# Kernel optimization log

Measured on AMD Instinct MI355X. Metric: run time of the kernel, lower is better.

## Reference

```python
import jax, jax.numpy as jnp
import numpy as np

D_MODEL = 1024
NUM_HEADS = 16
D_HEAD = D_MODEL // NUM_HEADS
BATCH = 4
SEQ = 2048
NEG_INF = -1e30


def setup_inputs() -> dict:
    key = jax.random.key(0)
    k_x, k_q, k_k, k_v, k_o = jax.random.split(key, 5)
    scale = 1.0 / np.sqrt(D_MODEL)
    x = jax.random.normal(k_x, (BATCH, SEQ, D_MODEL), dtype=jnp.float32)
    Qw = jax.random.normal(k_q, (D_MODEL, D_MODEL), dtype=jnp.float32) * scale
    Kw = jax.random.normal(k_k, (D_MODEL, D_MODEL), dtype=jnp.float32) * scale
    Vw = jax.random.normal(k_v, (D_MODEL, D_MODEL), dtype=jnp.float32) * scale
    Ow = jax.random.normal(k_o, (D_MODEL, D_MODEL), dtype=jnp.float32) * scale
    padding_mask = jnp.zeros((BATCH, SEQ), dtype=bool)  # True = masked position
    return {"x": x, "Qw": Qw, "Kw": Kw, "Vw": Vw, "Ow": Ow, "padding_mask": padding_mask}


def reference(x, Qw, Kw, Vw, Ow, padding_mask):
    B, S, D = x.shape
    H, dh = NUM_HEADS, D_HEAD
    # torch Linear (no bias): y = x @ W.T
    q = jnp.einsum("bsd,ed->bse", x, Qw).reshape(B, S, H, dh)
    k = jnp.einsum("bsd,ed->bse", x, Kw).reshape(B, S, H, dh)
    v = jnp.einsum("bsd,ed->bse", x, Vw).reshape(B, S, H, dh)
    # scores: [B, H, Sq, Sk]
    score = jnp.einsum("bqhd,bkhd->bhqk", q, k) / jnp.sqrt(jnp.float32(dh))
    # causal mask (masked=True)
    causal = jnp.tril(jnp.ones((S, S), dtype=bool))  # True = keep
    score = jnp.where(causal[None, None, :, :], score, NEG_INF)
    # padding mask: True = masked key position
    score = jnp.where(padding_mask[:, None, None, :], NEG_INF, score)
    attn = jax.nn.softmax(score, axis=-1)  # dropout=0.0 (eval mode)
    ctx = jnp.einsum("bhqk,bkhd->bqhd", attn, v).reshape(B, S, D)
    out = jnp.einsum("bsd,ed->bse", ctx, Ow)
    return out
```

## Files before the change

kernel.cpp:

```cpp
#include <hip/hip_runtime.h>
#include <hip/hip_bf16.h>

typedef __attribute__((ext_vector_type(8))) short short8;
typedef __attribute__((ext_vector_type(4))) float f32x4;

#define MFMA_BF16_16x16x32(a,b,c) __builtin_amdgcn_mfma_f32_16x16x32_bf16((a),(b),(c),0,0,0)

constexpr int B_  = 4;
constexpr int S_  = 2048;
constexpr int H_  = 16;
constexpr int DH_ = 64;
constexpr int D_  = 1024;
constexpr int M_  = B_ * S_;

__device__ __forceinline__ unsigned short f2bf(float f) {
  union { float f; unsigned u; } v; v.f = f;
  unsigned u = v.u;
  u += 0x7fffu + ((u >> 16) & 1u);
  return (unsigned short)(u >> 16);
}

__device__ __forceinline__ short8 cvt8(f32x4 a, f32x4 b) {
  union { __hip_bfloat162 h[4]; short8 s; } u;
  u.h[0] = __float22bfloat162_rn(make_float2(a[0], a[1]));
  u.h[1] = __float22bfloat162_rn(make_float2(a[2], a[3]));
  u.h[2] = __float22bfloat162_rn(make_float2(b[0], b[1]));
  u.h[3] = __float22bfloat162_rn(make_float2(b[2], b[3]));
  return u.s;
}

__global__ __launch_bounds__(256)
void gemm_qkv(const float* __restrict__ x,
              const float* __restrict__ Qw, const float* __restrict__ Kw,
              const float* __restrict__ Vw,
              unsigned short* __restrict__ Qo, unsigned short* __restrict__ Ko,
              unsigned short* __restrict__ VTo) {
  constexpr int BM = 128, BK = 32, LDK = 40;
  __shared__ __align__(16) short As[BM * LDK];
  __shared__ __align__(16) short Bs[BM * LDK];

  const int nb = blockIdx.x;
  const float* W;
  unsigned short* out;
  float scale = 1.0f;
  int epi;
  if (nb < 8)       { W = Qw; out = Qo;  scale = 0.125f; epi = 1; }
  else if (nb < 16) { W = Kw; out = Ko;  epi = 1; }
  else              { W = Vw; out = VTo; epi = 2; }

  const int tid  = threadIdx.x;
  const int lane = tid & 63;
  const int w    = tid >> 6;
  const int quad = lane >> 4;
  const int l16  = lane & 15;
  const int wm   = (w >> 1) * 64;
  const int wn   = (w & 1) * 64;

  const int m0 = blockIdx.y * BM;
  const int n0 = (nb & 7) * 128;

  f32x4 acc[4][4];
  #pragma unroll
  for (int i = 0; i < 4; ++i)
    #pragma unroll
    for (int j = 0; j < 4; ++j)
      acc[i][j] = (f32x4){0.f, 0.f, 0.f, 0.f};

  for (int k0 = 0; k0 < D_; k0 += BK) {
    __syncthreads();
    #pragma unroll
    for (int i = 0; i < 2; ++i) {
      int flat = i * 256 + tid;
      int row  = flat >> 2;
      int col  = (flat & 3) * 8;
      const float* Ap = x + (size_t)(m0 + row) * D_ + k0 + col;
      *(short8*)(&As[row * LDK + col]) = cvt8(*(const f32x4*)Ap, *(const f32x4*)(Ap + 4));
      const float* Wp = W + (size_t)(n0 + row) * D_ + k0 + col;
      *(short8*)(&Bs[row * LDK + col]) = cvt8(*(const f32x4*)Wp, *(const f32x4*)(Wp + 4));
    }
    __syncthreads();

    short8 af[4], bf[4];
    #pragma unroll
    for (int i = 0; i < 4; ++i)
      af[i] = *(const short8*)(&As[(wm + i * 16 + l16) * LDK + quad * 8]);
    #pragma unroll
    for (int j = 0; j < 4; ++j)
      bf[j] = *(const short8*)(&Bs[(wn + j * 16 + l16) * LDK + quad * 8]);
    #pragma unroll
    for (int i = 0; i < 4; ++i)
      #pragma unroll
      for (int j = 0; j < 4; ++j)
        acc[i][j] = MFMA_BF16_16x16x32(af[i], bf[j], acc[i][j]);
  }

  #pragma unroll
  for (int i = 0; i < 4; ++i)
    #pragma unroll
    for (int j = 0; j < 4; ++j)
      #pragma unroll
      for (int r = 0; r < 4; ++r) {
        int m = m0 + wm + i * 16 + quad * 4 + r;
        int n = n0 + wn + j * 16 + l16;
        unsigned short bv = f2bf(acc[i][j][r] * scale);
        int b = m >> 11, s = m & (S_ - 1);
        int h = n >> 6,  d = n & (DH_ - 1);
        if (epi == 1)
          out[((size_t)(b * H_ + h) * S_ + s) * DH_ + d] = bv;
        else
          out[((size_t)(b * H_ + h) * DH_ + d) * S_ + s] = bv;
      }
}

__global__ __launch_bounds__(256)
void gemm_out(const unsigned short* __restrict__ A,
              const float* __restrict__ W,
              float* __restrict__ out) {
  constexpr int BM = 128, BK = 32, LDK = 40;
  __shared__ __align__(16) short As[BM * LDK];
  __shared__ __align__(16) short Bs[BM * LDK];

  const int tid  = threadIdx.x;
  const int lane = tid & 63;
  const int w    = tid >> 6;
  const int quad = lane >> 4;
  const int l16  = lane & 15;
  const int wm   = (w >> 1) * 64;
  const int wn   = (w & 1) * 64;

  const int m0 = blockIdx.y * BM;
  const int n0 = blockIdx.x * 128;

  f32x4 acc[4][4];
  #pragma unroll
  for (int i = 0; i < 4; ++i)
    #pragma unroll
    for (int j = 0; j < 4; ++j)
      acc[i][j] = (f32x4){0.f, 0.f, 0.f, 0.f};

  for (int k0 = 0; k0 < D_; k0 += BK) {
    __syncthreads();
    #pragma unroll
    for (int i = 0; i < 2; ++i) {
      int flat = i * 256 + tid;
      int row  = flat >> 2;
      int col  = (flat & 3) * 8;
      *(short8*)(&As[row * LDK + col]) =
          *(const short8*)(A + (size_t)(m0 + row) * D_ + k0 + col);
      const float* Wp = W + (size_t)(n0 + row) * D_ + k0 + col;
      *(short8*)(&Bs[row * LDK + col]) = cvt8(*(const f32x4*)Wp, *(const f32x4*)(Wp + 4));
    }
    __syncthreads();

    short8 af[4], bf[4];
    #pragma unroll
    for (int i = 0; i < 4; ++i)
      af[i] = *(const short8*)(&As[(wm + i * 16 + l16) * LDK + quad * 8]);
    #pragma unroll
    for (int j = 0; j < 4; ++j)
      bf[j] = *(const short8*)(&Bs[(wn + j * 16 + l16) * LDK + quad * 8]);
    #pragma unroll
    for (int i = 0; i < 4; ++i)
      #pragma unroll
      for (int j = 0; j < 4; ++j)
        acc[i][j] = MFMA_BF16_16x16x32(af[i], bf[j], acc[i][j]);
  }

  #pragma unroll
  for (int i = 0; i < 4; ++i)
    #pragma unroll
    for (int j = 0; j < 4; ++j)
      #pragma unroll
      for (int r = 0; r < 4; ++r) {
        int m = m0 + wm + i * 16 + quad * 4 + r;
        int n = n0 + wn + j * 16 + l16;
        out[(size_t)m * D_ + n] = acc[i][j][r];
      }
}

__global__ __launch_bounds__(256)
void attn(const unsigned short* __restrict__ Q,
          const unsigned short* __restrict__ K,
          const unsigned short* __restrict__ VT,
          const unsigned char* __restrict__ pmask,
          unsigned short* __restrict__ CTX) {
  constexpr int LDP = 72;
  __shared__ __align__(16) short Ps[4 * 32 * LDP];

  const int tid  = threadIdx.x;
  const int lane = tid & 63;
  const int w    = tid >> 6;
  const int quad = lane >> 4;
  const int l16  = lane & 15;

  const int b    = blockIdx.z;
  const int h    = blockIdx.y;
  const int pair = blockIdx.x * 4 + w;

  const unsigned short* Qh = Q  + ((size_t)b * H_ + h) * S_ * DH_;
  const unsigned short* Kh = K  + ((size_t)b * H_ + h) * S_ * DH_;
  const unsigned short* Vh = VT + ((size_t)b * H_ + h) * DH_ * S_;
  const unsigned char* pmb = pmask + (size_t)b * S_;
  unsigned short* CTXb = CTX + (size_t)b * S_ * D_;
  short* Pw = &Ps[w * 32 * LDP];

  for (int half = 0; half < 2; ++half) {
    const int qt = half ? (63 - pair) : pair;
    const int qw = qt * 32;

    short8 qf[2][2];
    #pragma unroll
    for (int i = 0; i < 2; ++i)
      #pragma unroll
      for (int c = 0; c < 2; ++c)
        qf[i][c] = *(const short8*)(Qh + (size_t)(qw + i * 16 + l16) * DH_ + c * 32 + quad * 8);

    f32x4 acc[2][4];
    float mrow[2][4], lrow[2][4];
    #pragma unroll
    for (int i = 0; i < 2; ++i)
      #pragma unroll
      for (int t = 0; t < 4; ++t) acc[i][t] = (f32x4){0.f, 0.f, 0.f, 0.f};
    #pragma unroll
    for (int i = 0; i < 2; ++i)
      #pragma unroll
      for (int r = 0; r < 4; ++r) { mrow[i][r] = -1e30f; lrow[i][r] = 0.f; }

    const int ntiles = (qw >> 6) + 1;
    for (int kt = 0; kt < ntiles; ++kt) {
      const int k0 = kt * 64;

      unsigned char pd[4];
      #pragma unroll
      for (int t = 0; t < 4; ++t) pd[t] = pmb[k0 + t * 16 + l16];

      f32x4 sc[2][4];
      __builtin_amdgcn_s_setprio(1);
      #pragma unroll
      for (int t = 0; t < 4; ++t) {
        const unsigned short* kp = Kh + (size_t)(k0 + t * 16 + l16) * DH_ + quad * 8;
        short8 kb0 = *(const short8*)(kp);
        short8 kb1 = *(const short8*)(kp + 32);
        #pragma unroll
        for (int i = 0; i < 2; ++i) {
          f32x4 z = (f32x4){0.f, 0.f, 0.f, 0.f};
          z = MFMA_BF16_16x16x32(qf[i][0], kb0, z);
          sc[i][t] = MFMA_BF16_16x16x32(qf[i][1], kb1, z);
        }
      }
      __builtin_amdgcn_s_setprio(0);

      #pragma unroll
      for (int t = 0; t < 4; ++t) {
        int key = k0 + t * 16 + l16;
        bool pad = pd[t] != 0;
        #pragma unroll
        for (int i = 0; i < 2; ++i)
          #pragma unroll
          for (int r = 0; r < 4; ++r) {
            int qrow = qw + i * 16 + quad * 4 + r;
            if (pad || key > qrow) sc[i][t][r] = -1e30f;
          }
      }

      #pragma unroll
      for (int i = 0; i < 2; ++i)
        #pragma unroll
        for (int r = 0; r < 4; ++r) {
          float rm = fmaxf(fmaxf(sc[i][0][r], sc[i][1][r]), fmaxf(sc[i][2][r], sc[i][3][r]));
          #pragma unroll
          for (int off = 8; off; off >>= 1) rm = fmaxf(rm, __shfl_xor(rm, off, 16));
          float mnew = fmaxf(mrow[i][r], rm);
          float al = __expf(mrow[i][r] - mnew);
          float rs = 0.f;
          #pragma unroll
          for (int t = 0; t < 4; ++t) {
            float p = __expf(sc[i][t][r] - mnew);
            sc[i][t][r] = p;
            rs += p;
          }
          #pragma unroll
          for (int off = 8; off; off >>= 1) rs += __shfl_xor(rs, off, 16);
          lrow[i][r] = lrow[i][r] * al + rs;
          mrow[i][r] = mnew;
          #pragma unroll
          for (int t = 0; t < 4; ++t) acc[i][t][r] *= al;
        }

      #pragma unroll
      for (int i = 0; i < 2; ++i)
        #pragma unroll
        for (int t = 0; t < 4; ++t)
          #pragma unroll
          for (int r = 0; r < 4; ++r)
            Pw[(i * 16 + quad * 4 + r) * LDP + t * 16 + l16] = (short)f2bf(sc[i][t][r]);

      __builtin_amdgcn_s_setprio(1);
      #pragma unroll
      for (int ks = 0; ks < 2; ++ks) {
        short8 pa0 = *(const short8*)(&Pw[l16 * LDP + ks * 32 + quad * 8]);
        short8 pa1 = *(const short8*)(&Pw[(16 + l16) * LDP + ks * 32 + quad * 8]);
        #pragma unroll
        for (int t = 0; t < 4; ++t) {
          short8 vb = *(const short8*)(Vh + (size_t)(t * 16 + l16) * S_ + k0 + ks * 32 + quad * 8);
          acc[0][t] = MFMA_BF16_16x16x32(pa0, vb, acc[0][t]);
          acc[1][t] = MFMA_BF16_16x16x32(pa1, vb, acc[1][t]);
        }
      }
      __builtin_amdgcn_s_setprio(0);
    }

    #pragma unroll
    for (int i = 0; i < 2; ++i)
      #pragma unroll
      for (int r = 0; r < 4; ++r) {
        int qrow = qw + i * 16 + quad * 4 + r;
        float inv = 1.0f / lrow[i][r];
        #pragma unroll
        for (int t = 0; t < 4; ++t)
          CTXb[(size_t)qrow * D_ + h * DH_ + t * 16 + l16] = f2bf(acc[i][t][r] * inv);
      }
  }
}

extern "C" void kernel_launch(void* const* d_in, const int* in_sizes, int n_in,
                              void* d_out, int out_size, void* d_ws, size_t ws_size,
                              hipStream_t stream) {
  const float* x  = (const float*)d_in[0];
  const float* Qw = (const float*)d_in[1];
  const float* Kw = (const float*)d_in[2];
  const float* Vw = (const float*)d_in[3];
  const float* Ow = (const float*)d_in[4];
  const unsigned char* pm = (const unsigned char*)d_in[5];

  const size_t NE = (size_t)M_ * D_;
  unsigned short* Qall  = (unsigned short*)d_out;
  unsigned short* CTXa  = (unsigned short*)d_out + NE;
  unsigned short* Kall  = (unsigned short*)d_ws;
  unsigned short* VTall = (unsigned short*)d_ws + NE;

  gemm_qkv<<<dim3(24, M_ / 128), 256, 0, stream>>>(x, Qw, Kw, Vw,
                                                   Qall, Kall, VTall);

  attn<<<dim3(8, H_, B_), 256, 0, stream>>>(Qall, Kall, VTall, pm, CTXa);

  hipMemcpyAsync(d_ws, (const void*)CTXa, NE * sizeof(unsigned short),
                 hipMemcpyDeviceToDevice, stream);

  gemm_out<<<dim3(D_ / 128, M_ / 128), 256, 0, stream>>>((unsigned short*)d_ws,
                                                         Ow, (float*)d_out);
}
```

Baseline: 428.1 us.

## Prefetch K/V tiles in registers, remap blocks to XCDs, skip causal mask off-diagonal

Within the attention kernel, the K fragments for the next key tile are loaded into registers during the current iteration. All V fragments are loaded before the softmax, so global-load latency overlaps compute. The causal comparison now runs only on the diagonal tile, and the padding mask becomes an additive bias. The launch becomes a 1D grid that maps each (batch, head) onto one XCD, so the blocks sharing K/V hit the same L2. This raises register pressure, which may reduce occupancy.

```diff
diff --git a/kernel.cpp b/kernel.cpp
--- a/kernel.cpp
+++ b/kernel.cpp
@@ -193,9 +193,14 @@
   const int quad = lane >> 4;
   const int l16  = lane & 15;
 
-  const int b    = blockIdx.z;
-  const int h    = blockIdx.y;
-  const int pair = blockIdx.x * 4 + w;
+  const int L    = blockIdx.x;
+  const int xcd  = L & 7;
+  const int slot = L >> 3;
+  const int bh   = xcd + 8 * (slot & 7);
+  const int xp   = slot >> 3;
+  const int b    = bh >> 4;
+  const int h    = bh & 15;
+  const int pair = xp * 4 + w;
 
   const unsigned short* Qh = Q  + ((size_t)b * H_ + h) * S_ * DH_;
   const unsigned short* Kh = K  + ((size_t)b * H_ + h) * S_ * DH_;
@@ -227,8 +232,18 @@
       for (int r = 0; r < 4; ++r) { mrow[i][r] = -1e30f; lrow[i][r] = 0.f; }
 
     const int ntiles = (qw >> 6) + 1;
+
+    short8 kb[8];
+    #pragma unroll
+    for (int t = 0; t < 4; ++t) {
+      const unsigned short* kp = Kh + (size_t)(t * 16 + l16) * DH_ + quad * 8;
+      kb[t * 2]     = *(const short8*)(kp);
+      kb[t * 2 + 1] = *(const short8*)(kp + 32);
+    }
+
     for (int kt = 0; kt < ntiles; ++kt) {
       const int k0 = kt * 64;
+      const bool last = (kt == ntiles - 1);
 
       unsigned char pd[4];
       #pragma unroll
@@ -238,29 +253,54 @@
       __builtin_amdgcn_s_setprio(1);
       #pragma unroll
       for (int t = 0; t < 4; ++t) {
-        const unsigned short* kp = Kh + (size_t)(k0 + t * 16 + l16) * DH_ + quad * 8;
-        short8 kb0 = *(const short8*)(kp);
-        short8 kb1 = *(const short8*)(kp + 32);
         #pragma unroll
         for (int i = 0; i < 2; ++i) {
           f32x4 z = (f32x4){0.f, 0.f, 0.f, 0.f};
-          z = MFMA_BF16_16x16x32(qf[i][0], kb0, z);
-          sc[i][t] = MFMA_BF16_16x16x32(qf[i][1], kb1, z);
+          z = MFMA_BF16_16x16x32(qf[i][0], kb[t * 2], z);
+          sc[i][t] = MFMA_BF16_16x16x32(qf[i][1], kb[t * 2 + 1], z);
         }
       }
       __builtin_amdgcn_s_setprio(0);
 
-      #pragma unroll
-      for (int t = 0; t < 4; ++t) {
-        int key = k0 + t * 16 + l16;
-        bool pad = pd[t] != 0;
+      short8 vb[8];
+      #pragma unroll
+      for (int ks = 0; ks < 2; ++ks)
+        #pragma unroll
+        for (int t = 0; t < 4; ++t)
+          vb[ks * 4 + t] = *(const short8*)(Vh + (size_t)(t * 16 + l16) * S_ +
+                                            k0 + ks * 32 + quad * 8);
+      {
+        const int kn0 = (last ? k0 : k0 + 64);
+        #pragma unroll
+        for (int t = 0; t < 4; ++t) {
+          const unsigned short* kp = Kh + (size_t)(kn0 + t * 16 + l16) * DH_ + quad * 8;
+          kb[t * 2]     = *(const short8*)(kp);
+          kb[t * 2 + 1] = *(const short8*)(kp + 32);
+        }
+      }
+
+      float pb[4];
+      #pragma unroll
+      for (int t = 0; t < 4; ++t) pb[t] = pd[t] ? -1e30f : 0.f;
+      #pragma unroll
+      for (int t = 0; t < 4; ++t)
         #pragma unroll
         for (int i = 0; i < 2; ++i)
           #pragma unroll
-          for (int r = 0; r < 4; ++r) {
-            int qrow = qw + i * 16 + quad * 4 + r;
-            if (pad || key > qrow) sc[i][t][r] = -1e30f;
-          }
+          for (int r = 0; r < 4; ++r)
+            sc[i][t][r] += pb[t];
+      if (last) {
+        #pragma unroll
+        for (int t = 0; t < 4; ++t) {
+          int key = k0 + t * 16 + l16;
+          #pragma unroll
+          for (int i = 0; i < 2; ++i)
+            #pragma unroll
+            for (int r = 0; r < 4; ++r) {
+              int qrow = qw + i * 16 + quad * 4 + r;
+              if (key > qrow) sc[i][t][r] = -1e30f;
+            }
+        }
       }
 
       #pragma unroll
@@ -302,9 +342,8 @@
         short8 pa1 = *(const short8*)(&Pw[(16 + l16) * LDP + ks * 32 + quad * 8]);
         #pragma unroll
         for (int t = 0; t < 4; ++t) {
-          short8 vb = *(const short8*)(Vh + (size_t)(t * 16 + l16) * S_ + k0 + ks * 32 + quad * 8);
-          acc[0][t] = MFMA_BF16_16x16x32(pa0, vb, acc[0][t]);
-          acc[1][t] = MFMA_BF16_16x16x32(pa1, vb, acc[1][t]);
+          acc[0][t] = MFMA_BF16_16x16x32(pa0, vb[ks * 4 + t], acc[0][t]);
+          acc[1][t] = MFMA_BF16_16x16x32(pa1, vb[ks * 4 + t], acc[1][t]);
         }
       }
       __builtin_amdgcn_s_setprio(0);
@@ -342,7 +381,7 @@
   gemm_qkv<<<dim3(24, M_ / 128), 256, 0, stream>>>(x, Qw, Kw, Vw,
                                                    Qall, Kall, VTall);
 
-  attn<<<dim3(8, H_, B_), 256, 0, stream>>>(Qall, Kall, VTall, pm, CTXa);
+  attn<<<dim3(512), 256, 0, stream>>>(Qall, Kall, VTall, pm, CTXa);
 
   hipMemcpyAsync(d_ws, (const void*)CTXa, NE * sizeof(unsigned short),
                  hipMemcpyDeviceToDevice, stream);
```

New measurement: 424.1 us. No clear change (-0.9%).
